# Kernel optimization log

Hardware: AMD Instinct MI355X
Metric: run time of the kernel (lower is better)

The kernel has to match this reference:

```python
import jax, jax.numpy as jnp
import numpy as np

BSZ, ILEN, TLEN = 64, 256, 64
IDIM, HDIM, ODIM = 512, 1024, 128


def setup_inputs() -> dict:
    key = jax.random.key(0)
    k1, k2, k3, k4 = jax.random.split(key, 4)
    # xavier-uniform-like scales (exact init values don't matter for correctness)
    def xavier(k, shape):
        fan_in, fan_out = shape[1], shape[0]
        lim = (6.0 / (fan_in + fan_out)) ** 0.5
        return jax.random.uniform(k, shape, jnp.float32, -lim, lim)
    return {
        "inp": jax.random.normal(k1, (BSZ, ILEN, IDIM), jnp.float32),
        "tlen": TLEN,
        "w_ih": xavier(k2, (4 * HDIM, IDIM)),
        "w_hh": xavier(k3, (4 * HDIM, HDIM)),
        "b": jnp.zeros((4 * HDIM,), jnp.float32),
        "clf_w": xavier(k4, (ODIM, HDIM)),
        "clf_b": jnp.zeros((ODIM,), jnp.float32),
    }


def _lstm_forward(inp, tlen, w_ih, w_hh, b, clf_w, clf_b):
    bsz, ilen, _ = inp.shape
    hdim = w_hh.shape[1]
    # pad tlen zero timesteps at the end (matches F.pad [0,0,0,tlen])
    inp_padded = jnp.pad(inp, ((0, 0), (0, tlen), (0, 0)))
    # precompute input projection for all timesteps: [B, T, 4H]
    x_proj = jnp.einsum("bti,gi->btg", inp_padded, w_ih) + b
    x_proj_t = jnp.swapaxes(x_proj, 0, 1)  # [T, B, 4H]

    def step(carry, xg):
        h, c = carry
        gates = xg + h @ w_hh.T  # [B, 4H]
        i, f, g, o = jnp.split(gates, 4, axis=-1)
        i = jax.nn.sigmoid(i)
        f = jax.nn.sigmoid(f)
        g = jnp.tanh(g)
        o = jax.nn.sigmoid(o)
        c_new = f * c + i * g
        h_new = o * jnp.tanh(c_new)
        return (h_new, c_new), h_new

    h0 = jnp.zeros((bsz, hdim), inp.dtype)
    c0 = jnp.zeros((bsz, hdim), inp.dtype)
    _, hs = jax.lax.scan(step, (h0, c0), x_proj_t)  # hs: [T, B, H]
    hs = jnp.swapaxes(hs, 0, 1)  # [B, T, H]
    probs = jax.nn.sigmoid(jnp.einsum("bth,oh->bto", hs, clf_w) + clf_b)
    return probs[:, ilen:]


def reference(inp, tlen, w_ih, w_hh, b, clf_w, clf_b):
    return _lstm_forward(inp, tlen, w_ih, w_hh, b, clf_w, clf_b)
```

## Files before the change

### kernel.cpp

```cpp
#include <hip/hip_runtime.h>
#include <hip/hip_bf16.h>

#define BSZ  64
#define ILEN 256
#define TLEN 64
#define TTOT (ILEN + TLEN)
#define IDIM 512
#define HDIM 1024
#define ODIM 128

#define NBLK 256
#define NTHR 512
#define NGRP 8
#define GBLK 32
#define UPB  32
#define NT   8
#define PN   132
#define HSLOT (BSZ * HDIM)
#define XBUFF (2 * 8 * 4 * 32)

typedef __attribute__((ext_vector_type(8))) short short8;
typedef __attribute__((ext_vector_type(4))) float f32x4;
typedef _Float16 half_t;

__device__ inline ushort f2bf(float f) {
  unsigned u = __builtin_bit_cast(unsigned, f);
  u += 0x7fffu + ((u >> 16) & 1u);
  return (ushort)(u >> 16);
}

__device__ inline float fast_sigmoid(float x) {
  float e = __expf(-x);
  return 1.0f / (1.0f + e);
}
__device__ inline float fast_tanh(float x) {
  float e = __expf(2.0f * x);
  return 1.0f - 2.0f / (1.0f + e);
}

__device__ inline void st_h_sys(ushort* p, ushort v) {
  __hip_atomic_store(p, v, __ATOMIC_RELAXED, __HIP_MEMORY_SCOPE_SYSTEM);
}
__device__ inline void vm_drain() { asm volatile("s_waitcnt vmcnt(0)" ::: "memory"); }

template<bool FAST>
__device__ __forceinline__ int ldflag(const int* p) {
  if constexpr (FAST)
    return __hip_atomic_load(p, __ATOMIC_RELAXED, __HIP_MEMORY_SCOPE_AGENT);
  else
    return __hip_atomic_load(p, __ATOMIC_RELAXED, __HIP_MEMORY_SCOPE_SYSTEM);
}
template<bool FAST>
__device__ __forceinline__ void stflag(int* p, int v) {
  if constexpr (FAST)
    __hip_atomic_store(p, v, __ATOMIC_RELAXED, __HIP_MEMORY_SCOPE_AGENT);
  else
    __hip_atomic_store(p, v, __ATOMIC_RELAXED, __HIP_MEMORY_SCOPE_SYSTEM);
}

template<bool FAST>
__device__ __forceinline__ void ld_h4(const ushort* p, short8& a0, short8& a1,
                                      short8& a2, short8& a3) {
  if constexpr (FAST)
    asm volatile("global_load_dwordx4 %0, %4, off sc0\n\t"
                 "global_load_dwordx4 %1, %4, off offset:64 sc0\n\t"
                 "global_load_dwordx4 %2, %4, off offset:128 sc0\n\t"
                 "global_load_dwordx4 %3, %4, off offset:192 sc0\n\t"
                 "s_waitcnt vmcnt(0)"
                 : "=&v"(a0), "=&v"(a1), "=&v"(a2), "=&v"(a3)
                 : "v"(p) : "memory");
  else
    asm volatile("global_load_dwordx4 %0, %4, off sc0 sc1\n\t"
                 "global_load_dwordx4 %1, %4, off offset:64 sc0 sc1\n\t"
                 "global_load_dwordx4 %2, %4, off offset:128 sc0 sc1\n\t"
                 "global_load_dwordx4 %3, %4, off offset:192 sc0 sc1\n\t"
                 "s_waitcnt vmcnt(0)"
                 : "=&v"(a0), "=&v"(a1), "=&v"(a2), "=&v"(a3)
                 : "v"(p) : "memory");
}

__device__ __forceinline__ void gload_lds16(const ushort* g, ushort* l) {
  __builtin_amdgcn_global_load_lds(
      (const __attribute__((address_space(1))) unsigned int*)g,
      (__attribute__((address_space(3))) unsigned int*)l, 16, 0, 0);
}

__global__ void prep_kernel(const float* __restrict__ inp, const float* __restrict__ clfw,
                            const float* __restrict__ w_ih, const float* __restrict__ w_hh,
                            ushort* __restrict__ inp_bf, ushort* __restrict__ clfw_bf,
                            ushort* __restrict__ wih_bf, ushort* __restrict__ whh_sw,
                            ushort* __restrict__ hbuf, int* __restrict__ bar,
                            int* __restrict__ hand)
{
  const long np  = (long)gridDim.x * blockDim.x;
  const long tid = (long)blockIdx.x * blockDim.x + threadIdx.x;

  const float4* in4 = (const float4*)inp;
  ushort4* ob4 = (ushort4*)inp_bf;
  for (long i = tid; i < (long)BSZ * ILEN * IDIM / 4; i += np) {
    float4 v = in4[i];
    ushort4 o; o.x = f2bf(v.x); o.y = f2bf(v.y); o.z = f2bf(v.z); o.w = f2bf(v.w);
    ob4[i] = o;
  }
  const float4* cw4 = (const float4*)clfw;
  ushort4* cb4 = (ushort4*)clfw_bf;
  for (long i = tid; i < (long)ODIM * HDIM / 4; i += np) {
    float4 v = cw4[i];
    ushort4 o; o.x = f2bf(v.x); o.y = f2bf(v.y); o.z = f2bf(v.z); o.w = f2bf(v.w);
    cb4[i] = o;
  }
  const float4* wi4 = (const float4*)w_ih;
  ushort4* wb4 = (ushort4*)wih_bf;
  for (long i = tid; i < (long)4 * HDIM * IDIM / 4; i += np) {
    float4 v = wi4[i];
    ushort4 o; o.x = f2bf(v.x); o.y = f2bf(v.y); o.z = f2bf(v.z); o.w = f2bf(v.w);
    wb4[i] = o;
  }
  for (long f = tid; f < 32L * 8 * 4 * 8 * 64; f += np) {
    const int lane = (int)(f & 63);
    const int nt   = (int)((f >> 6) & 7);
    const int c    = (int)((f >> 9) & 3);
    const int wv   = (int)((f >> 11) & 7);
    const int r    = (int)(f >> 14);
    const int nl   = nt * 16 + (lane & 15);
    const long grow = (long)(nl >> 5) * HDIM + r * UPB + (nl & 31);
    const int k = wv * 128 + c * 32 + (lane >> 4) * 8;
    const float* src = w_hh + grow * HDIM + k;
    const float4 s0 = *(const float4*)(src);
    const float4 s1 = *(const float4*)(src + 4);
    ushort4 d0, d1;
    d0.x = f2bf(s0.x); d0.y = f2bf(s0.y); d0.z = f2bf(s0.z); d0.w = f2bf(s0.w);
    d1.x = f2bf(s1.x); d1.y = f2bf(s1.y); d1.z = f2bf(s1.z); d1.w = f2bf(s1.w);
    ushort* dst = whh_sw + f * 8;
    *(ushort4*)(dst)     = d0;
    *(ushort4*)(dst + 4) = d1;
  }
  for (long i = tid; i < (long)4 * HSLOT; i += np)
    st_h_sys(hbuf + i, 0);
  for (long i = tid; i < NBLK * 32; i += np)
    __hip_atomic_store(bar + (int)i, 0, __ATOMIC_RELAXED, __HIP_MEMORY_SCOPE_SYSTEM);
  for (long i = tid; i < 256; i += np)
    __hip_atomic_store(hand + (int)i, 0, __ATOMIC_RELAXED, __HIP_MEMORY_SCOPE_SYSTEM);
}

__global__ __launch_bounds__(256, 2) void xproj_kernel(
    const ushort* __restrict__ inp_bf, const ushort* __restrict__ wih_bf,
    half_t* __restrict__ xproj)
{
  __shared__ ushort As[128 * 32];
  __shared__ ushort Bs[128 * 32];

  const int tid = threadIdx.x;
  const int wv = tid >> 6, lane = tid & 63, l15 = lane & 15, quad = lane >> 4;
  const int bs = (blockIdx.x & 7) * 512 + (blockIdx.x >> 3);
  const long mb = (long)(bs >> 5) * 128;
  const long nb = (long)(bs & 31) * 128;
  const int wr = wv >> 1, wc = wv & 1;

  const int srow = wv * 32 + (lane >> 2);
  const int scol = (lane & 3) * 8;
  const ushort* ga = inp_bf + (mb + srow) * IDIM + scol;
  const ushort* gb = wih_bf + (nb + srow) * IDIM + scol;
  ushort* const la = As + wv * 32 * 32;
  ushort* const lb = Bs + wv * 32 * 32;

  f32x4 acc[4][4];
  #pragma unroll
  for (int mt = 0; mt < 4; ++mt)
    #pragma unroll
    for (int nt = 0; nt < 4; ++nt)
      #pragma unroll
      for (int r = 0; r < 4; ++r) acc[mt][nt][r] = 0.0f;

  for (int kc = 0; kc < IDIM / 32; ++kc) {
    const int k = kc * 32;
    gload_lds16(ga + k,             la);
    gload_lds16(ga + 16 * IDIM + k, la + 16 * 32);
    gload_lds16(gb + k,             lb);
    gload_lds16(gb + 16 * IDIM + k, lb + 16 * 32);
    asm volatile("s_waitcnt vmcnt(0)" ::: "memory");
    __syncthreads();

    short8 af[4], bf[4];
    #pragma unroll
    for (int mt = 0; mt < 4; ++mt)
      af[mt] = *(const short8*)(As + (wr * 64 + mt * 16 + l15) * 32 + quad * 8);
    #pragma unroll
    for (int nt = 0; nt < 4; ++nt)
      bf[nt] = *(const short8*)(Bs + (wc * 64 + nt * 16 + l15) * 32 + quad * 8);
    #pragma unroll
    for (int mt = 0; mt < 4; ++mt)
      #pragma unroll
      for (int nt = 0; nt < 4; ++nt)
        acc[mt][nt] = __builtin_amdgcn_mfma_f32_16x16x32_bf16(af[mt], bf[nt],
                                                              acc[mt][nt], 0, 0, 0);
    __syncthreads();
  }

  #pragma unroll
  for (int mt = 0; mt < 4; ++mt)
    #pragma unroll
    for (int nt = 0; nt < 4; ++nt)
      #pragma unroll
      for (int r = 0; r < 4; ++r) {
        const long m = mb + wr * 64 + mt * 16 + quad * 4 + r;
        const long n = nb + wc * 64 + nt * 16 + l15;
        xproj[m * (4 * HDIM) + n] = (half_t)acc[mt][nt][r];
      }
}

template<bool FAST>
__device__ __forceinline__ void lstm_body(
    const ushort* __restrict__ whh_sw, const half_t* __restrict__ xproj,
    const float* __restrict__ bias, ushort* __restrict__ hbuf,
    ushort* __restrict__ hs_bf, int* __restrict__ flags)
{
  extern __shared__ float part[];
  float* const xbuf = part + 8 * 16 * PN;

  const int tid  = threadIdx.x;
  const int wv   = tid >> 6;
  const int lane = tid & 63;
  const int l15  = lane & 15;
  const int quad = lane >> 4;
  const int blk  = blockIdx.x;
  const int g    = blk & 7;
  const int role = blk >> 3;
  const int j0u  = role * UPB;
  const int m0   = g * 8;

  short8 wfrag[4][NT];
  {
    const ushort* wp = whh_sw + (long)(role * 8 + wv) * 16384 + lane * 8;
    #pragma unroll
    for (int c = 0; c < 4; ++c)
      #pragma unroll
      for (int nt = 0; nt < NT; ++nt)
        wfrag[c][nt] = *(const short8*)(wp + (c * NT + nt) * 512);
  }
  #pragma unroll
  for (int c = 0; c < 4; ++c)
    #pragma unroll
    for (int nt = 0; nt < NT; ++nt)
      asm volatile("" : "+v"(wfrag[c][nt]));

  const int em = tid >> 5;
  const int uu = tid & 31;
  float bi = 0, bf_ = 0, bg = 0, bo = 0;
  if (tid < 256) {
    bi  = bias[0 * HDIM + j0u + uu];
    bf_ = bias[1 * HDIM + j0u + uu];
    bg  = bias[2 * HDIM + j0u + uu];
    bo  = bias[3 * HDIM + j0u + uu];
  }
  float cst = 0.0f;

  const int lane4 = (tid - 256) & 255;
  const int em4 = lane4 >> 5;
  const int g4  = (lane4 >> 3) & 3;
  const int u0  = (lane4 & 7) * 4;
  const half_t* xsrc = xproj + (long)(m0 + em4) * ILEN * (4 * HDIM)
                       + g4 * HDIM + j0u + u0;

  int* const fmine = flags + (g * GBLK + role) * 32;
  const int fidx = (lane < 4) ? (g * GBLK + wv * 4 + lane) : (g * GBLK + role);
  const int* const myfp = flags + fidx * 32;

  if (tid >= 256) {
    ushort4 x0 = *(const ushort4*)xsrc;
    float4 v;
    v.x = (float)__builtin_bit_cast(half_t, (ushort)x0.x);
    v.y = (float)__builtin_bit_cast(half_t, (ushort)x0.y);
    v.z = (float)__builtin_bit_cast(half_t, (ushort)x0.z);
    v.w = (float)__builtin_bit_cast(half_t, (ushort)x0.w);
    *(float4*)(xbuf + 0 * 1024 + em4 * 128 + g4 * 32 + u0) = v;
  }

  for (int t = 0; t < TTOT; ++t) {
    const ushort* __restrict__ hsrc = hbuf + (t & 3) * HSLOT;
    ushort* __restrict__ hdst = hbuf + ((t + 1) & 3) * HSLOT;

    for (;;) {
      int v = ldflag<FAST>(myfp);
      if (__all(v >= t)) break;
      __builtin_amdgcn_s_sleep(1);
    }

    const ushort* hb = hsrc + (long)(m0 + (l15 & 7)) * HDIM + wv * 128 + quad * 8;
    short8 ah0, ah1, ah2, ah3;
    ld_h4<FAST>(hb, ah0, ah1, ah2, ah3);

    ushort4 xr;
    const bool havex = (tid >= 256) && (t + 1 < ILEN);
    if (havex) {
      const ushort* xp = (const ushort*)(xsrc + (long)(t + 1) * (4 * HDIM));
      asm volatile("global_load_dwordx2 %0, %1, off"
                   : "=&v"(xr) : "v"(xp) : "memory");
    }

    f32x4 acc[NT];
    #pragma unroll
    for (int nt = 0; nt < NT; ++nt)
      #pragma unroll
      for (int r = 0; r < 4; ++r) acc[nt][r] = 0.0f;

    #pragma unroll
    for (int nt = 0; nt < NT; ++nt)
      acc[nt] = __builtin_amdgcn_mfma_f32_16x16x32_bf16(ah0, wfrag[0][nt], acc[nt], 0, 0, 0);
    #pragma unroll
    for (int nt = 0; nt < NT; ++nt)
      acc[nt] = __builtin_amdgcn_mfma_f32_16x16x32_bf16(ah1, wfrag[1][nt], acc[nt], 0, 0, 0);
    #pragma unroll
    for (int nt = 0; nt < NT; ++nt)
      acc[nt] = __builtin_amdgcn_mfma_f32_16x16x32_bf16(ah2, wfrag[2][nt], acc[nt], 0, 0, 0);
    #pragma unroll
    for (int nt = 0; nt < NT; ++nt)
      acc[nt] = __builtin_amdgcn_mfma_f32_16x16x32_bf16(ah3, wfrag[3][nt], acc[nt], 0, 0, 0);

    if (quad < 2) {
      #pragma unroll
      for (int nt = 0; nt < NT; ++nt)
        #pragma unroll
        for (int r = 0; r < 4; ++r)
          part[(wv * 16 + quad * 4 + r) * PN + nt * 16 + l15] = acc[nt][r];
    }

    asm volatile("s_waitcnt lgkmcnt(0)" ::: "memory");
    __builtin_amdgcn_s_barrier();

    ushort h16 = 0;
    if (tid < 256) {
      float xi = 0, xf = 0, xg = 0, xo = 0;
      if (t < ILEN) {
        const float* xb = xbuf + (t & 1) * 1024 + em * 128 + uu;
        xi = xb[0]; xf = xb[32]; xg = xb[64]; xo = xb[96];
      }
      float gi = bi + xi, gf = bf_ + xf, gg = bg + xg, go = bo + xo;
      #pragma unroll
      for (int w = 0; w < 8; ++w) {
        const float* pw = part + (w * 16 + em) * PN;
        gi += pw[0 * 32 + uu];
        gf += pw[1 * 32 + uu];
        gg += pw[2 * 32 + uu];
        go += pw[3 * 32 + uu];
      }
      const float si = fast_sigmoid(gi);
      const float sf = fast_sigmoid(gf);
      const float tg = fast_tanh(gg);
      const float so = fast_sigmoid(go);
      cst = sf * cst + si * tg;
      const float h = so * fast_tanh(cst);
      h16 = f2bf(h);
      if constexpr (FAST)
        hdst[(long)(m0 + em) * HDIM + j0u + uu] = h16;
      else
        st_h_sys(hdst + (long)(m0 + em) * HDIM + j0u + uu, h16);
    } else if (havex) {
      asm volatile("s_waitcnt vmcnt(0)" ::: "memory");
      float4 v;
      v.x = (float)__builtin_bit_cast(half_t, (ushort)xr.x);
      v.y = (float)__builtin_bit_cast(half_t, (ushort)xr.y);
      v.z = (float)__builtin_bit_cast(half_t, (ushort)xr.z);
      v.w = (float)__builtin_bit_cast(half_t, (ushort)xr.w);
      *(float4*)(xbuf + ((t + 1) & 1) * 1024 + em4 * 128 + g4 * 32 + u0) = v;
    }

    vm_drain();
    __syncthreads();
    if (tid == 0) stflag<FAST>(fmine, t + 1);

    if (tid < 256 && t >= ILEN)
      hs_bf[((long)(m0 + em) * TLEN + (t - ILEN)) * HDIM + j0u + uu] = h16;
  }
}

__global__ __launch_bounds__(NTHR, 2) void lstm_kernel(
    const ushort* __restrict__ whh_sw, const half_t* __restrict__ xproj,
    const float* __restrict__ bias,
    ushort* __restrict__ hbuf, ushort* __restrict__ hs_bf,
    int* __restrict__ flags, int* __restrict__ hand)
{
  int xcd = 0;
  asm volatile("s_getreg_b32 %0, hwreg(HW_REG_XCC_ID)" : "=s"(xcd));
  const int g = blockIdx.x & 7;
  if (threadIdx.x == 0) {
    __hip_atomic_fetch_or(&hand[g * 8], 1 << (xcd & 7),
                          __ATOMIC_RELAXED, __HIP_MEMORY_SCOPE_SYSTEM);
    __hip_atomic_fetch_add(&hand[64 + g * 8], 1,
                           __ATOMIC_RELAXED, __HIP_MEMORY_SCOPE_SYSTEM);
  }
  while (__hip_atomic_load(&hand[64 + g * 8], __ATOMIC_RELAXED,
                           __HIP_MEMORY_SCOPE_SYSTEM) < GBLK)
    __builtin_amdgcn_s_sleep(2);
  const bool fast =
      __popc(__hip_atomic_load(&hand[g * 8], __ATOMIC_RELAXED,
                               __HIP_MEMORY_SCOPE_SYSTEM)) == 1;

  if (fast) lstm_body<true >(whh_sw, xproj, bias, hbuf, hs_bf, flags);
  else      lstm_body<false>(whh_sw, xproj, bias, hbuf, hs_bf, flags);
}

__global__ __launch_bounds__(256, 1) void clf_kernel(
    const ushort* __restrict__ hs_bf, const ushort* __restrict__ clfw_bf,
    const float* __restrict__ clf_b, float* __restrict__ out)
{
  const int tid = threadIdx.x;
  const int wv = tid >> 6, lane = tid & 63, l15 = lane & 15, quad = lane >> 4;
  const int m0 = blockIdx.x * 64 + wv * 16;

  f32x4 acc[8];
  #pragma unroll
  for (int nt = 0; nt < 8; ++nt)
    #pragma unroll
    for (int r = 0; r < 4; ++r) acc[nt][r] = 0.0f;

  for (int kc = 0; kc < HDIM / 32; ++kc) {
    const int k = kc * 32 + quad * 8;
    short8 a = *(const short8*)(hs_bf + (long)(m0 + l15) * HDIM + k);
    #pragma unroll
    for (int nt = 0; nt < 8; ++nt) {
      short8 b = *(const short8*)(clfw_bf + (long)(nt * 16 + l15) * HDIM + k);
      acc[nt] = __builtin_amdgcn_mfma_f32_16x16x32_bf16(a, b, acc[nt], 0, 0, 0);
    }
  }
  #pragma unroll
  for (int nt = 0; nt < 8; ++nt) {
    const int n = nt * 16 + l15;
    const float bn = clf_b[n];
    #pragma unroll
    for (int r = 0; r < 4; ++r) {
      const int m = m0 + quad * 4 + r;
      out[(long)m * ODIM + n] = fast_sigmoid(acc[nt][r] + bn);
    }
  }
}

extern "C" void kernel_launch(void* const* d_in, const int* in_sizes, int n_in,
                              void* d_out, int out_size, void* d_ws, size_t ws_size,
                              hipStream_t stream) {
  const float* inp   = (const float*)d_in[0];
  const float* w_ih  = (const float*)d_in[2];
  const float* w_hh  = (const float*)d_in[3];
  const float* bias  = (const float*)d_in[4];
  const float* clf_w = (const float*)d_in[5];
  const float* clf_b = (const float*)d_in[6];
  float* out = (float*)d_out;

  char* ws = (char*)d_ws;
  ushort* inp_bf  = (ushort*)(ws + 0);
  ushort* wih_bf  = (ushort*)(ws + 16777216);
  ushort* whh_sw  = (ushort*)(ws + 20971520);
  ushort* clfw_bf = (ushort*)(ws + 29360128);
  ushort* hbuf    = (ushort*)(ws + 29622272);
  ushort* hs_bf   = (ushort*)(ws + 30146560);
  int*    bar     = (int*)   (ws + 38535168);
  int*    hand    = (int*)   (ws + 38567936);
  half_t* xproj   = (half_t*)(ws + 38568960);

  prep_kernel<<<4096, 256, 0, stream>>>(inp, clf_w, w_ih, w_hh,
                                        inp_bf, clfw_bf, wih_bf, whh_sw,
                                        hbuf, bar, hand);
  xproj_kernel<<<4096, 256, 0, stream>>>(inp_bf, wih_bf, xproj);
  lstm_kernel<<<NBLK, NTHR, (8 * 16 * PN + XBUFF) * 4, stream>>>(
      whh_sw, xproj, bias, hbuf, hs_bf, bar, hand);
  clf_kernel<<<64, 256, 0, stream>>>(hs_bf, clfw_bf, clf_b, out);
}
```

Measured before the change: 1.066 ms.

## Assign LSTM groups by XCD at runtime so each group stays on one die

Each block now takes its (group, role) from an atomic per-XCD counter, so all 32 blocks of a batch group land on the same XCD where possible and can use the fast same-die flag and h-buffer path. Blocks beyond 32 on an XCD fill the leftover slots through a global overflow counter, which needs a grid-wide barrier before the assignment is known. Flag polling also skips a block's own flag, so fewer lanes load. The cost is a global startup barrier and a dependence on blocks being spread across XCDs as assumed.

Result: slower. 1.205 ms (+13.0%).

```diff
diff --git a/kernel.cpp b/kernel.cpp
--- a/kernel.cpp
+++ b/kernel.cpp
@@ -213,7 +213,8 @@
 __device__ __forceinline__ void lstm_body(
     const ushort* __restrict__ whh_sw, const half_t* __restrict__ xproj,
     const float* __restrict__ bias, ushort* __restrict__ hbuf,
-    ushort* __restrict__ hs_bf, int* __restrict__ flags)
+    ushort* __restrict__ hs_bf, int* __restrict__ flags,
+    const int g, const int role)
 {
   extern __shared__ float part[];
   float* const xbuf = part + 8 * 16 * PN;
@@ -223,9 +224,6 @@
   const int lane = tid & 63;
   const int l15  = lane & 15;
   const int quad = lane >> 4;
-  const int blk  = blockIdx.x;
-  const int g    = blk & 7;
-  const int role = blk >> 3;
   const int j0u  = role * UPB;
   const int m0   = g * 8;
 
@@ -263,8 +261,9 @@
                        + g4 * HDIM + j0u + u0;
 
   int* const fmine = flags + (g * GBLK + role) * 32;
-  const int fidx = (lane < 4) ? (g * GBLK + wv * 4 + lane) : (g * GBLK + role);
-  const int* const myfp = flags + fidx * 32;
+  const int prole = wv * 4 + (lane & 3);
+  const bool pollme = (lane < 4) && (prole != role);
+  const int* const myfp = flags + (g * GBLK + prole) * 32;
 
   if (tid >= 256) {
     ushort4 x0 = *(const ushort4*)xsrc;
@@ -281,7 +280,8 @@
     ushort* __restrict__ hdst = hbuf + ((t + 1) & 3) * HSLOT;
 
     for (;;) {
-      int v = ldflag<FAST>(myfp);
+      int v = 0x7fffffff;
+      if (pollme) v = ldflag<FAST>(myfp);
       if (__all(v >= t)) break;
       __builtin_amdgcn_s_sleep(1);
     }
@@ -380,24 +380,47 @@
     ushort* __restrict__ hbuf, ushort* __restrict__ hs_bf,
     int* __restrict__ flags, int* __restrict__ hand)
 {
-  int xcd = 0;
-  asm volatile("s_getreg_b32 %0, hwreg(HW_REG_XCC_ID)" : "=s"(xcd));
-  const int g = blockIdx.x & 7;
+  __shared__ int s_g, s_role, s_fast;
   if (threadIdx.x == 0) {
-    __hip_atomic_fetch_or(&hand[g * 8], 1 << (xcd & 7),
-                          __ATOMIC_RELAXED, __HIP_MEMORY_SCOPE_SYSTEM);
-    __hip_atomic_fetch_add(&hand[64 + g * 8], 1,
-                           __ATOMIC_RELAXED, __HIP_MEMORY_SCOPE_SYSTEM);
-  }
-  while (__hip_atomic_load(&hand[64 + g * 8], __ATOMIC_RELAXED,
-                           __HIP_MEMORY_SCOPE_SYSTEM) < GBLK)
-    __builtin_amdgcn_s_sleep(2);
-  const bool fast =
-      __popc(__hip_atomic_load(&hand[g * 8], __ATOMIC_RELAXED,
-                               __HIP_MEMORY_SCOPE_SYSTEM)) == 1;
-
-  if (fast) lstm_body<true >(whh_sw, xproj, bias, hbuf, hs_bf, flags);
-  else      lstm_body<false>(whh_sw, xproj, bias, hbuf, hs_bf, flags);
+    int xcd = 0;
+    asm volatile("s_getreg_b32 %0, hwreg(HW_REG_XCC_ID)" : "=s"(xcd));
+    xcd &= 7;
+    const int idx = __hip_atomic_fetch_add(&hand[xcd], 1,
+                        __ATOMIC_RELAXED, __HIP_MEMORY_SCOPE_SYSTEM);
+    int ov = -1;
+    if (idx >= GBLK)
+      ov = __hip_atomic_fetch_add(&hand[9], 1,
+               __ATOMIC_RELAXED, __HIP_MEMORY_SCOPE_SYSTEM);
+    __hip_atomic_fetch_add(&hand[8], 1,
+        __ATOMIC_RELEASE, __HIP_MEMORY_SCOPE_SYSTEM);
+    while (__hip_atomic_load(&hand[8], __ATOMIC_ACQUIRE,
+                             __HIP_MEMORY_SCOPE_SYSTEM) < NBLK)
+      __builtin_amdgcn_s_sleep(2);
+    int cnt[8];
+    #pragma unroll
+    for (int x = 0; x < 8; ++x)
+      cnt[x] = __hip_atomic_load(&hand[x], __ATOMIC_RELAXED,
+                                 __HIP_MEMORY_SCOPE_SYSTEM);
+    int g, role;
+    if (idx < GBLK) {
+      g = xcd; role = idx;
+    } else {
+      int r = ov; g = 0; role = 0;
+      for (int x = 0; x < 8; ++x) {
+        const int have = cnt[x] < GBLK ? cnt[x] : GBLK;
+        const int def = GBLK - have;
+        if (r < def) { g = x; role = have + r; break; }
+        r -= def;
+      }
+    }
+    s_g = g; s_role = role; s_fast = (cnt[g] >= GBLK) ? 1 : 0;
+  }
+  __syncthreads();
+  const int g = s_g, role = s_role;
+  const bool fast = s_fast != 0;
+
+  if (fast) lstm_body<true >(whh_sw, xproj, bias, hbuf, hs_bf, flags, g, role);
+  else      lstm_body<false>(whh_sw, xproj, bias, hbuf, hs_bf, flags, g, role);
 }
 
 __global__ __launch_bounds__(256, 1) void clf_kernel(
```
